# Kernel optimization log

Hardware: AMD Instinct MI355X
Metric: run time of the kernel (lower is better)

## Reference

```python
import jax, jax.numpy as jnp
import numpy as np

T, N, E = 12, 100000, 3200000
F = H = 64
O, L = 32, 2


def setup_inputs() -> dict:
    key = jax.random.key(0)
    ks = jax.random.split(key, 13)
    sc = 0.08  # keep gate pre-activations in a sane range
    return {
        "x": jax.random.normal(ks[0], (T, N, F), jnp.float32),
        "hidden_states": jax.random.normal(ks[1], (L, N, H), jnp.float32),
        "cell_states": jax.random.normal(ks[2], (L, N, H), jnp.float32),
        "Wx_self": jax.random.normal(ks[3], (L, 4, F, H), jnp.float32) * sc,
        "Wx_neigh": jax.random.normal(ks[4], (L, 4, F, H), jnp.float32) * sc,
        "Wh_self": jax.random.normal(ks[5], (L, 4, H, H), jnp.float32) * sc,
        "Wh_neigh": jax.random.normal(ks[6], (L, 4, H, H), jnp.float32) * sc,
        "w_c": jax.random.normal(ks[7], (L, 3, H), jnp.float32) * sc,  # peephole i,f,o
        "bias": jax.random.normal(ks[8], (L, 4, H), jnp.float32) * sc,  # i,f,c,o
        "Wout": jax.random.normal(ks[9], (H, O), jnp.float32) * sc,
        "bout": jax.random.normal(ks[10], (O,), jnp.float32) * sc,
        "src": jax.random.randint(ks[11], (E,), 0, N, jnp.int32),
        "dst": jax.random.randint(ks[12], (E,), 0, N, jnp.int32),
    }


def reference(x, hidden_states, cell_states, Wx_self, Wx_neigh, Wh_self,
              Wh_neigh, w_c, bias, Wout, bout, src, dst):
    # mean aggregation over incoming edges (DGL copy_u + mean reduce)
    deg = jax.ops.segment_sum(jnp.ones((E,), x.dtype), dst, num_segments=N)
    deg_inv = jnp.where(deg > 0, 1.0 / deg, 0.0)[:, None]  # [N,1]

    def mean_agg(feat):  # [N,D] -> [N,D]
        return jax.ops.segment_sum(feat[src], dst, num_segments=N) * deg_inv

    def gates(feat, agg, Ws, Wn):  # Ws,Wn: [4,D,H] -> [4,N,H]
        return (jnp.einsum('nf,gfh->gnh', feat, Ws)
                + jnp.einsum('nf,gfh->gnh', agg, Wn))

    def step(carry, x_t):
        hs, cs = carry  # [L,N,H] each
        inp = x_t
        new_h, new_c = [], []
        for j in range(L):
            h, c = hs[j], cs[j]
            x_agg = mean_agg(inp)  # reuse_msg_passing: one agg shared by 4 gates
            h_agg = mean_agg(h)
            pre = gates(inp, x_agg, Wx_self[j], Wx_neigh[j]) \
                + gates(h, h_agg, Wh_self[j], Wh_neigh[j])  # [4,N,H]
            i = jax.nn.sigmoid(pre[0] + w_c[j, 0] * c + bias[j, 0])
            f = jax.nn.sigmoid(pre[1] + w_c[j, 1] * c + bias[j, 1])
            c_tilde = jnp.tanh(pre[2] + bias[j, 2])
            nc = f * c + i * c_tilde
            o = jax.nn.sigmoid(pre[3] + w_c[j, 2] * nc + bias[j, 3])
            nh = o * jnp.tanh(nc)
            new_h.append(nh)
            new_c.append(nc)
            inp = nh
        out_t = inp @ Wout + bout  # [N,O]
        return (jnp.stack(new_h), jnp.stack(new_c)), out_t

    (h_f, c_f), outs = jax.lax.scan(step, (hidden_states, cell_states), x)
    return outs, h_f, c_f  # outs: [T,N,O]
```

## Files before the change

kernel.cpp:

```cpp
#include <hip/hip_runtime.h>

#define T_STEPS 12
#define NN 100000
#define EE 3200000
#define HD 64
#define OD 32
#define NBK 391

typedef __attribute__((ext_vector_type(8))) short short8;
typedef __attribute__((ext_vector_type(4))) float f32x4;
typedef __attribute__((ext_vector_type(2))) float f32x2;
typedef unsigned short u16;
typedef unsigned char u8;

__device__ __forceinline__ u16 f2b(float x) {
  union { float f; unsigned u; } v; v.f = x;
  unsigned r = v.u + 0x7FFFu + ((v.u >> 16) & 1u);
  return (u16)(r >> 16);
}
__device__ __forceinline__ float sigm(float x) {
  x = fminf(fmaxf(x, -30.f), 30.f);
  return 1.0f / (1.0f + __expf(-x));
}
__device__ __forceinline__ float tanh_f(float x) {
  x = fminf(fmaxf(x, -15.f), 15.f);
  float e = __expf(2.0f * x);
  return (e - 1.0f) / (e + 1.0f);
}

__device__ __forceinline__ uint2 pack8_fp8(const float* f) {
  unsigned lo = 0, hi = 0;
  lo = __builtin_amdgcn_cvt_pk_fp8_f32(f[0], f[1], lo, false);
  lo = __builtin_amdgcn_cvt_pk_fp8_f32(f[2], f[3], lo, true);
  hi = __builtin_amdgcn_cvt_pk_fp8_f32(f[4], f[5], hi, false);
  hi = __builtin_amdgcn_cvt_pk_fp8_f32(f[6], f[7], hi, true);
  return make_uint2(lo, hi);
}
__device__ __forceinline__ u8 f2q(float x) {
  return (u8)(__builtin_amdgcn_cvt_pk_fp8_f32(x, 0.f, 0u, false) & 0xFFu);
}
__device__ __forceinline__ void acc8_fp8(uint2 v, float* a) {
  f32x2 p0 = __builtin_amdgcn_cvt_pk_f32_fp8(v.x, false);
  f32x2 p1 = __builtin_amdgcn_cvt_pk_f32_fp8(v.x, true);
  f32x2 p2 = __builtin_amdgcn_cvt_pk_f32_fp8(v.y, false);
  f32x2 p3 = __builtin_amdgcn_cvt_pk_f32_fp8(v.y, true);
  a[0] += p0[0]; a[1] += p0[1]; a[2] += p1[0]; a[3] += p1[1];
  a[4] += p2[0]; a[5] += p2[1]; a[6] += p3[0]; a[7] += p3[1];
}
__device__ __forceinline__ void dec16_acc(uint4 q, float* a) {
  f32x2 t;
  t = __builtin_amdgcn_cvt_pk_f32_fp8(q.x, false); a[0] += t[0]; a[1] += t[1];
  t = __builtin_amdgcn_cvt_pk_f32_fp8(q.x, true);  a[2] += t[0]; a[3] += t[1];
  t = __builtin_amdgcn_cvt_pk_f32_fp8(q.y, false); a[4] += t[0]; a[5] += t[1];
  t = __builtin_amdgcn_cvt_pk_f32_fp8(q.y, true);  a[6] += t[0]; a[7] += t[1];
  t = __builtin_amdgcn_cvt_pk_f32_fp8(q.z, false); a[8] += t[0]; a[9] += t[1];
  t = __builtin_amdgcn_cvt_pk_f32_fp8(q.z, true);  a[10] += t[0]; a[11] += t[1];
  t = __builtin_amdgcn_cvt_pk_f32_fp8(q.w, false); a[12] += t[0]; a[13] += t[1];
  t = __builtin_amdgcn_cvt_pk_f32_fp8(q.w, true);  a[14] += t[0]; a[15] += t[1];
}
__device__ __forceinline__ short8 s8_from_fp8(uint2 q) {
  f32x2 p0 = __builtin_amdgcn_cvt_pk_f32_fp8(q.x, false);
  f32x2 p1 = __builtin_amdgcn_cvt_pk_f32_fp8(q.x, true);
  f32x2 p2 = __builtin_amdgcn_cvt_pk_f32_fp8(q.y, false);
  f32x2 p3 = __builtin_amdgcn_cvt_pk_f32_fp8(q.y, true);
  short8 o;
  o[0] = (short)f2b(p0[0]); o[1] = (short)f2b(p0[1]);
  o[2] = (short)f2b(p1[0]); o[3] = (short)f2b(p1[1]);
  o[4] = (short)f2b(p2[0]); o[5] = (short)f2b(p2[1]);
  o[6] = (short)f2b(p3[0]); o[7] = (short)f2b(p3[1]);
  return o;
}
__device__ __forceinline__ short8 s8_from_f32(float4 a, float4 b) {
  short8 o;
  o[0] = (short)f2b(a.x); o[1] = (short)f2b(a.y);
  o[2] = (short)f2b(a.z); o[3] = (short)f2b(a.w);
  o[4] = (short)f2b(b.x); o[5] = (short)f2b(b.y);
  o[6] = (short)f2b(b.z); o[7] = (short)f2b(b.w);
  return o;
}

__global__ __launch_bounds__(256) void k_bhist(const int* __restrict__ dst,
                                               int* __restrict__ bcnt, int E) {
  __shared__ int h[NBK];
  for (int i = threadIdx.x; i < NBK; i += 256) h[i] = 0;
  __syncthreads();
  int base = blockIdx.x * 4096;
#pragma unroll
  for (int i = 0; i < 16; ++i) {
    int e = base + i * 256 + threadIdx.x;
    if (e < E) atomicAdd(&h[dst[e] >> 8], 1);
  }
  __syncthreads();
  for (int i = threadIdx.x; i < NBK; i += 256)
    if (h[i]) atomicAdd(&bcnt[i], h[i]);
}

__global__ __launch_bounds__(512) void k_bscan(const int* __restrict__ bcnt,
                                               int* __restrict__ bcur) {
  __shared__ int buf[512];
  int tid = threadIdx.x;
  int v = (tid < NBK) ? bcnt[tid] : 0;
  buf[tid] = v;
  __syncthreads();
  for (int off = 1; off < 512; off <<= 1) {
    int t = (tid >= off) ? buf[tid - off] : 0;
    __syncthreads();
    buf[tid] += t;
    __syncthreads();
  }
  if (tid < NBK) bcur[tid] = buf[tid] - v;
}

__global__ __launch_bounds__(256) void k_bscatter(const int* __restrict__ src,
                                                  const int* __restrict__ dst,
                                                  int* __restrict__ bcur,
                                                  uint2* __restrict__ binned, int E) {
  __shared__ int h[NBK];
  __shared__ int base[NBK];
  __shared__ int cur[NBK];
  for (int i = threadIdx.x; i < NBK; i += 256) { h[i] = 0; cur[i] = 0; }
  __syncthreads();
  int b0 = blockIdx.x * 4096;
  int d[16], s[16];
#pragma unroll
  for (int i = 0; i < 16; ++i) {
    int e = b0 + i * 256 + threadIdx.x;
    if (e < E) {
      d[i] = dst[e];
      s[i] = src[e];
      atomicAdd(&h[d[i] >> 8], 1);
    } else d[i] = -1;
  }
  __syncthreads();
  for (int i = threadIdx.x; i < NBK; i += 256)
    if (h[i]) base[i] = atomicAdd(&bcur[i], h[i]);
  __syncthreads();
#pragma unroll
  for (int i = 0; i < 16; ++i) {
    if (d[i] >= 0) {
      int bk = d[i] >> 8;
      int r = atomicAdd(&cur[bk], 1);
      binned[base[bk] + r] = make_uint2((unsigned)s[i], (unsigned)d[i]);
    }
  }
}

__global__ __launch_bounds__(256) void k_count2(const uint2* __restrict__ binned,
                                                int* __restrict__ deg, int E) {
  int e = blockIdx.x * 256 + threadIdx.x;
  if (e < E) atomicAdd(&deg[binned[e].y], 1);
}

__global__ __launch_bounds__(1024) void k_scanA(const int* __restrict__ deg,
                                                int* __restrict__ excl,
                                                int* __restrict__ btot, int n) {
  __shared__ int buf[1024];
  int tid = threadIdx.x;
  int i = blockIdx.x * 1024 + tid;
  int v = (i < n) ? deg[i] : 0;
  buf[tid] = v;
  __syncthreads();
  for (int off = 1; off < 1024; off <<= 1) {
    int t = (tid >= off) ? buf[tid - off] : 0;
    __syncthreads();
    buf[tid] += t;
    __syncthreads();
  }
  if (i < n) excl[i] = buf[tid] - v;
  if (tid == 1023) btot[blockIdx.x] = buf[1023];
}

__global__ __launch_bounds__(128) void k_scanB(const int* __restrict__ btot,
                                               int* __restrict__ boffs, int nb) {
  __shared__ int buf[128];
  int tid = threadIdx.x;
  int v = (tid < nb) ? btot[tid] : 0;
  buf[tid] = v;
  __syncthreads();
  for (int off = 1; off < 128; off <<= 1) {
    int t = (tid >= off) ? buf[tid - off] : 0;
    __syncthreads();
    buf[tid] += t;
    __syncthreads();
  }
  if (tid < nb) boffs[tid] = buf[tid] - v;
}

__global__ __launch_bounds__(1024) void k_scanC(const int* __restrict__ deg,
                                                const int* __restrict__ excl,
                                                const int* __restrict__ boffs,
                                                int* __restrict__ row_ptr,
                                                int* __restrict__ cursor,
                                                float* __restrict__ deg_inv, int n) {
  int i = blockIdx.x * 1024 + threadIdx.x;
  if (i < n) {
    int v = excl[i] + boffs[blockIdx.x];
    int d = deg[i];
    row_ptr[i] = v;
    cursor[i] = v;
    deg_inv[i] = d ? (1.0f / (float)d) : 0.0f;
    if (i == n - 1) row_ptr[n] = v + d;
  }
}

__global__ __launch_bounds__(256) void k_scatter2(const uint2* __restrict__ binned,
                                                  int* __restrict__ cursor,
                                                  int* __restrict__ csr, int E) {
  int e = blockIdx.x * 256 + threadIdx.x;
  if (e < E) {
    uint2 p = binned[e];
    int pos = atomicAdd(&cursor[p.y], 1);
    csr[pos] = (int)p.x;
  }
}

__global__ __launch_bounds__(256) void k_prep(const float* __restrict__ Wxs,
                                              const float* __restrict__ Wxn,
                                              const float* __restrict__ Whs,
                                              const float* __restrict__ Whn,
                                              u16* __restrict__ bprep) {
  int idx = blockIdx.x * 256 + threadIdx.x;
  int l = idx >> 16;
  int kb = (idx >> 13) & 7;
  int fi = (idx >> 9) & 15;
  int ln = (idx >> 3) & 63;
  int j = idx & 7;
  int fc = kb * 32 + ((ln >> 4) << 3) + j;
  int g = fi & 3;
  int kk = ((fi >> 2) << 4) + (ln & 15);
  int t = fc >> 6, f = fc & 63;
  const float* tabs[4] = {Wxs, Wxn, Whs, Whn};
  bprep[idx] = f2b(tabs[t][((size_t)(l * 4 + g) * 64 + f) * 64 + kk]);
}

__global__ __launch_bounds__(256) void k_prepw(const float* __restrict__ Wout,
                                               u16* __restrict__ wp) {
  int idx = blockIdx.x * 256 + threadIdx.x;
  int kb = idx >> 10;
  int fi = (idx >> 9) & 1;
  int ln = (idx >> 3) & 63;
  int j = idx & 7;
  int k = kb * 32 + ((ln >> 4) << 3) + j;
  int o = fi * 16 + (ln & 15);
  wp[idx] = f2b(Wout[k * 32 + o]);
}

__global__ __launch_bounds__(256) void k_convxall(const float* __restrict__ x,
                                                  u8* __restrict__ XQ) {
  int tid = blockIdx.x * 256 + threadIdx.x;
  int j = tid & 7;
  int tn = tid >> 3;
  int n = tn % NN;
  int t = tn / NN;
  const float* rp = x + (size_t)tn * 64 + j * 8;
  float4 v0 = *reinterpret_cast<const float4*>(rp);
  float4 v1 = *reinterpret_cast<const float4*>(rp + 4);
  float f[8] = {v0.x, v0.y, v0.z, v0.w, v1.x, v1.y, v1.z, v1.w};
  *reinterpret_cast<uint2*>(XQ + (size_t)n * 768 + t * 64 + j * 8) = pack8_fp8(f);
}

__global__ __launch_bounds__(256) void k_inith(const float* __restrict__ h0,
                                               u16* __restrict__ H0bf,
                                               u16* __restrict__ L1bf,
                                               u8* __restrict__ HQ) {
  int idx = blockIdx.x * 256 + threadIdx.x;
  int n = idx >> 3, j = idx & 7;
#pragma unroll
  for (int L = 0; L < 2; ++L) {
    const float* rp = h0 + (size_t)L * NN * 64 + (size_t)n * 64 + j * 8;
    float4 v0 = *reinterpret_cast<const float4*>(rp);
    float4 v1 = *reinterpret_cast<const float4*>(rp + 4);
    float f[8] = {v0.x, v0.y, v0.z, v0.w, v1.x, v1.y, v1.z, v1.w};
    short8 o;
#pragma unroll
    for (int i = 0; i < 8; ++i) o[i] = (short)f2b(f[i]);
    if (L == 0)
      *reinterpret_cast<short8*>(H0bf + (size_t)n * 64 + j * 8) = o;
    else
      *reinterpret_cast<short8*>(L1bf + (size_t)n * 64 + j * 8) = o;
    *reinterpret_cast<uint2*>(HQ + (size_t)n * 128 + L * 64 + j * 8) = pack8_fp8(f);
  }
}

__global__ __launch_bounds__(256) void k_aggx(const u8* __restrict__ XQ,
                                              const int* __restrict__ row_ptr,
                                              const int* __restrict__ csr,
                                              const float* __restrict__ deg_inv,
                                              u8* __restrict__ AGGXq) {
  int node = blockIdx.x * 4 + (threadIdx.x >> 6);
  int lane = threadIdx.x & 63;
  int g = lane >> 4, m = lane & 15;
  int start = row_ptr[node], end = row_ptr[node + 1];
  float acc[3][16];
#pragma unroll
  for (int p = 0; p < 3; ++p)
#pragma unroll
    for (int i = 0; i < 16; ++i) acc[p][i] = 0.f;
  int e = start + g;
  for (; e + 4 < end; e += 8) {
    int s0 = csr[e], s1 = csr[e + 4];
    const u8* r0 = XQ + (size_t)s0 * 768 + m * 16;
    const u8* r1 = XQ + (size_t)s1 * 768 + m * 16;
#pragma unroll
    for (int p = 0; p < 3; ++p) {
      uint4 q0 = *reinterpret_cast<const uint4*>(r0 + p * 256);
      uint4 q1 = *reinterpret_cast<const uint4*>(r1 + p * 256);
      dec16_acc(q0, acc[p]);
      dec16_acc(q1, acc[p]);
    }
  }
  if (e < end) {
    int s0 = csr[e];
    const u8* r0 = XQ + (size_t)s0 * 768 + m * 16;
#pragma unroll
    for (int p = 0; p < 3; ++p) {
      uint4 q0 = *reinterpret_cast<const uint4*>(r0 + p * 256);
      dec16_acc(q0, acc[p]);
    }
  }
#pragma unroll
  for (int off = 16; off < 64; off <<= 1)
#pragma unroll
    for (int p = 0; p < 3; ++p)
#pragma unroll
      for (int i = 0; i < 16; ++i) acc[p][i] += __shfl_xor(acc[p][i], off);
  if (g == 0) {
    float sc = deg_inv[node];
#pragma unroll
    for (int p = 0; p < 3; ++p) {
      float f[16];
#pragma unroll
      for (int i = 0; i < 16; ++i) f[i] = acc[p][i] * sc;
      uint4 o;
      unsigned w;
      w = 0; w = __builtin_amdgcn_cvt_pk_fp8_f32(f[0], f[1], w, false);
      w = __builtin_amdgcn_cvt_pk_fp8_f32(f[2], f[3], w, true); o.x = w;
      w = 0; w = __builtin_amdgcn_cvt_pk_fp8_f32(f[4], f[5], w, false);
      w = __builtin_amdgcn_cvt_pk_fp8_f32(f[6], f[7], w, true); o.y = w;
      w = 0; w = __builtin_amdgcn_cvt_pk_fp8_f32(f[8], f[9], w, false);
      w = __builtin_amdgcn_cvt_pk_fp8_f32(f[10], f[11], w, true); o.z = w;
      w = 0; w = __builtin_amdgcn_cvt_pk_fp8_f32(f[12], f[13], w, false);
      w = __builtin_amdgcn_cvt_pk_fp8_f32(f[14], f[15], w, true); o.w = w;
      int t = p * 4 + (m >> 2);
      *reinterpret_cast<uint4*>(AGGXq + ((size_t)t * NN + node) * 64 + (m & 3) * 16) = o;
    }
  }
}

__global__ __launch_bounds__(256) void k_agg_pair(const u8* __restrict__ Q,
                                                  const int* __restrict__ row_ptr,
                                                  const int* __restrict__ csr,
                                                  const float* __restrict__ deg_inv,
                                                  u16* __restrict__ outp) {
  int node = blockIdx.x * 4 + (threadIdx.x >> 6);
  int lane = threadIdx.x & 63;
  int g = lane >> 4, m = lane & 15;
  int start = row_ptr[node], end = row_ptr[node + 1];
  float a[8] = {0, 0, 0, 0, 0, 0, 0, 0};
  int e = start + g;
  for (; e + 12 < end; e += 16) {
    int s0 = csr[e], s1 = csr[e + 4], s2 = csr[e + 8], s3 = csr[e + 12];
    uint2 v0 = *reinterpret_cast<const uint2*>(Q + (size_t)s0 * 128 + m * 8);
    uint2 v1 = *reinterpret_cast<const uint2*>(Q + (size_t)s1 * 128 + m * 8);
    uint2 v2 = *reinterpret_cast<const uint2*>(Q + (size_t)s2 * 128 + m * 8);
    uint2 v3 = *reinterpret_cast<const uint2*>(Q + (size_t)s3 * 128 + m * 8);
    acc8_fp8(v0, a); acc8_fp8(v1, a); acc8_fp8(v2, a); acc8_fp8(v3, a);
  }
  if (e + 4 < end) {
    int s0 = csr[e], s1 = csr[e + 4];
    uint2 v0 = *reinterpret_cast<const uint2*>(Q + (size_t)s0 * 128 + m * 8);
    uint2 v1 = *reinterpret_cast<const uint2*>(Q + (size_t)s1 * 128 + m * 8);
    acc8_fp8(v0, a); acc8_fp8(v1, a);
    e += 8;
  }
  if (e < end) {
    int s0 = csr[e];
    uint2 v0 = *reinterpret_cast<const uint2*>(Q + (size_t)s0 * 128 + m * 8);
    acc8_fp8(v0, a);
  }
#pragma unroll
  for (int off = 16; off < 64; off <<= 1) {
#pragma unroll
    for (int i = 0; i < 8; ++i) a[i] += __shfl_xor(a[i], off);
  }
  if (g == 0) {
    float sc = deg_inv[node];
    short8 o;
#pragma unroll
    for (int i = 0; i < 8; ++i) o[i] = (short)f2b(a[i] * sc);
    *reinterpret_cast<short8*>(outp + (size_t)node * 128 + m * 8) = o;
  }
}

__global__ __launch_bounds__(256, 2) void k_gates0(
    const float* __restrict__ xin, const u8* __restrict__ aggxq,
    u16* __restrict__ h0bf, const u16* __restrict__ agghl,
    u8* __restrict__ hq, float* __restrict__ cst, float* __restrict__ hf32,
    const u16* __restrict__ bprepl,
    const float* __restrict__ wcl, const float* __restrict__ biasl,
    int n_nodes, int writef32) {
  const int tid = threadIdx.x;
  const int lane = tid & 63;
  const int w = tid >> 6;
  const int nb = blockIdx.x * 64;
  const int cl = lane & 15;
  const int kg = lane >> 4;

  short8 breg[8][4];
#pragma unroll
  for (int kb = 0; kb < 8; ++kb)
#pragma unroll
    for (int fl = 0; fl < 4; ++fl)
      breg[kb][fl] = *reinterpret_cast<const short8*>(
          bprepl + (kb << 13) + (((w << 2) + fl) << 9) + (lane << 3));

  int gnc[4];
#pragma unroll
  for (int rg = 0; rg < 4; ++rg) {
    int g = nb + rg * 16 + cl;
    gnc[rg] = (g < n_nodes) ? g : (n_nodes - 1);
  }

  f32x4 acc[4][4];
  f32x4 z4 = {0.f, 0.f, 0.f, 0.f};
#pragma unroll
  for (int a = 0; a < 4; ++a)
#pragma unroll
    for (int b = 0; b < 4; ++b) acc[a][b] = z4;

  const int koff = kg << 3;
#pragma unroll
  for (int kb = 0; kb < 8; ++kb) {
    const int idx = ((kb & 1) << 5) + koff;
#pragma unroll
    for (int rg = 0; rg < 4; ++rg) {
      short8 a;
      if (kb < 2) {
        const float* rp = xin + (size_t)gnc[rg] * 64 + idx;
        a = s8_from_f32(*reinterpret_cast<const float4*>(rp),
                        *reinterpret_cast<const float4*>(rp + 4));
      } else if (kb < 4) {
        a = s8_from_fp8(*reinterpret_cast<const uint2*>(aggxq + (size_t)gnc[rg] * 64 + idx));
      } else if (kb < 6) {
        a = *reinterpret_cast<const short8*>(h0bf + (size_t)gnc[rg] * 64 + idx);
      } else {
        a = *reinterpret_cast<const short8*>(agghl + (size_t)gnc[rg] * 128 + idx);
      }
      acc[rg][0] = __builtin_amdgcn_mfma_f32_16x16x32_bf16(a, breg[kb][0], acc[rg][0], 0, 0, 0);
      acc[rg][1] = __builtin_amdgcn_mfma_f32_16x16x32_bf16(a, breg[kb][1], acc[rg][1], 0, 0, 0);
      acc[rg][2] = __builtin_amdgcn_mfma_f32_16x16x32_bf16(a, breg[kb][2], acc[rg][2], 0, 0, 0);
      acc[rg][3] = __builtin_amdgcn_mfma_f32_16x16x32_bf16(a, breg[kb][3], acc[rg][3], 0, 0, 0);
    }
  }

  const int k = (w << 4) + cl;
  const float wci = wcl[k], wcf = wcl[64 + k], wco = wcl[128 + k];
  const float bi = biasl[k], bfg = biasl[64 + k], bc = biasl[128 + k], bo = biasl[192 + k];
#pragma unroll
  for (int rg = 0; rg < 4; ++rg) {
#pragma unroll
    for (int r = 0; r < 4; ++r) {
      int n = nb + rg * 16 + kg * 4 + r;
      if (n < n_nodes) {
        size_t off = (size_t)n * 64 + k;
        float c_old = cst[off];
        float ig = sigm(acc[rg][0][r] + wci * c_old + bi);
        float fg = sigm(acc[rg][1][r] + wcf * c_old + bfg);
        float ct = tanh_f(acc[rg][2][r] + bc);
        float nc = fg * c_old + ig * ct;
        float og = sigm(acc[rg][3][r] + wco * nc + bo);
        float nh = og * tanh_f(nc);
        cst[off] = nc;
        h0bf[off] = f2b(nh);
        hq[(size_t)n * 128 + k] = f2q(nh);
        if (writef32) hf32[off] = nh;
      }
    }
  }
}

__global__ __launch_bounds__(256, 2) void k_gates1(
    const u16* __restrict__ h0bf, const u16* __restrict__ agghl,
    u16* __restrict__ l1bf, u8* __restrict__ hq,
    float* __restrict__ cst, float* __restrict__ hf32,
    const u16* __restrict__ bprepl,
    const float* __restrict__ wcl, const float* __restrict__ biasl,
    const u16* __restrict__ wproj, const float* __restrict__ boutp,
    float* __restrict__ outp, int n_nodes, int writef32) {
  __shared__ u16 Hsm[64 * 64];
  const int tid = threadIdx.x;
  const int lane = tid & 63;
  const int w = tid >> 6;
  const int nb = blockIdx.x * 64;
  const int cl = lane & 15;
  const int kg = lane >> 4;

  short8 breg[8][4];
#pragma unroll
  for (int kb = 0; kb < 8; ++kb)
#pragma unroll
    for (int fl = 0; fl < 4; ++fl)
      breg[kb][fl] = *reinterpret_cast<const short8*>(
          bprepl + (kb << 13) + (((w << 2) + fl) << 9) + (lane << 3));

  int gnc[4];
#pragma unroll
  for (int rg = 0; rg < 4; ++rg) {
    int g = nb + rg * 16 + cl;
    gnc[rg] = (g < n_nodes) ? g : (n_nodes - 1);
  }

  f32x4 acc[4][4];
  f32x4 z4 = {0.f, 0.f, 0.f, 0.f};
#pragma unroll
  for (int a = 0; a < 4; ++a)
#pragma unroll
    for (int b = 0; b < 4; ++b) acc[a][b] = z4;

  const int koff = kg << 3;
#pragma unroll
  for (int kb = 0; kb < 8; ++kb) {
    const int idx = ((kb & 1) << 5) + koff;
#pragma unroll
    for (int rg = 0; rg < 4; ++rg) {
      short8 a;
      if (kb < 2) {
        a = *reinterpret_cast<const short8*>(h0bf + (size_t)gnc[rg] * 64 + idx);
      } else if (kb < 4) {
        a = *reinterpret_cast<const short8*>(agghl + (size_t)gnc[rg] * 128 + idx);
      } else if (kb < 6) {
        a = *reinterpret_cast<const short8*>(l1bf + (size_t)gnc[rg] * 64 + idx);
      } else {
        a = *reinterpret_cast<const short8*>(agghl + (size_t)gnc[rg] * 128 + 64 + idx);
      }
      acc[rg][0] = __builtin_amdgcn_mfma_f32_16x16x32_bf16(a, breg[kb][0], acc[rg][0], 0, 0, 0);
      acc[rg][1] = __builtin_amdgcn_mfma_f32_16x16x32_bf16(a, breg[kb][1], acc[rg][1], 0, 0, 0);
      acc[rg][2] = __builtin_amdgcn_mfma_f32_16x16x32_bf16(a, breg[kb][2], acc[rg][2], 0, 0, 0);
      acc[rg][3] = __builtin_amdgcn_mfma_f32_16x16x32_bf16(a, breg[kb][3], acc[rg][3], 0, 0, 0);
    }
  }

  const int k = (w << 4) + cl;
  const float wci = wcl[k], wcf = wcl[64 + k], wco = wcl[128 + k];
  const float bi = biasl[k], bfg = biasl[64 + k], bc = biasl[128 + k], bo = biasl[192 + k];
#pragma unroll
  for (int rg = 0; rg < 4; ++rg) {
#pragma unroll
    for (int r = 0; r < 4; ++r) {
      int n = nb + rg * 16 + kg * 4 + r;
      if (n < n_nodes) {
        size_t off = (size_t)n * 64 + k;
        float c_old = cst[off];
        float ig = sigm(acc[rg][0][r] + wci * c_old + bi);
        float fg = sigm(acc[rg][1][r] + wcf * c_old + bfg);
        float ct = tanh_f(acc[rg][2][r] + bc);
        float nc = fg * c_old + ig * ct;
        float og = sigm(acc[rg][3][r] + wco * nc + bo);
        float nh = og * tanh_f(nc);
        cst[off] = nc;
        u16 hb = f2b(nh);
        l1bf[off] = hb;
        hq[(size_t)n * 128 + 64 + k] = f2q(nh);
        Hsm[(rg * 16 + kg * 4 + r) * 64 + k] = hb;
        if (writef32) hf32[off] = nh;
      }
    }
  }

  __syncthreads();
  short8 bw[2][2];
#pragma unroll
  for (int kb = 0; kb < 2; ++kb)
#pragma unroll
    for (int fi = 0; fi < 2; ++fi)
      bw[kb][fi] = *reinterpret_cast<const short8*>(wproj + (((kb * 2 + fi) * 64 + lane) << 3));
  short8 a0 = *reinterpret_cast<const short8*>(&Hsm[(w * 16 + cl) * 64 + kg * 8]);
  short8 a1 = *reinterpret_cast<const short8*>(&Hsm[(w * 16 + cl) * 64 + 32 + kg * 8]);
  f32x4 p0 = z4, p1 = z4;
  p0 = __builtin_amdgcn_mfma_f32_16x16x32_bf16(a0, bw[0][0], p0, 0, 0, 0);
  p0 = __builtin_amdgcn_mfma_f32_16x16x32_bf16(a1, bw[1][0], p0, 0, 0, 0);
  p1 = __builtin_amdgcn_mfma_f32_16x16x32_bf16(a0, bw[0][1], p1, 0, 0, 0);
  p1 = __builtin_amdgcn_mfma_f32_16x16x32_bf16(a1, bw[1][1], p1, 0, 0, 0);
  const float bo0 = boutp[cl], bo1 = boutp[16 + cl];
#pragma unroll
  for (int r = 0; r < 4; ++r) {
    int n = nb + w * 16 + kg * 4 + r;
    if (n < n_nodes) {
      outp[(size_t)n * OD + cl] = p0[r] + bo0;
      outp[(size_t)n * OD + 16 + cl] = p1[r] + bo1;
    }
  }
}

extern "C" void kernel_launch(void* const* d_in, const int* in_sizes, int n_in,
                              void* d_out, int out_size, void* d_ws, size_t ws_size,
                              hipStream_t stream) {
  const float* x = (const float*)d_in[0];
  const float* h0 = (const float*)d_in[1];
  const float* c0 = (const float*)d_in[2];
  const float* Wxs = (const float*)d_in[3];
  const float* Wxn = (const float*)d_in[4];
  const float* Whs = (const float*)d_in[5];
  const float* Whn = (const float*)d_in[6];
  const float* wc = (const float*)d_in[7];
  const float* bias = (const float*)d_in[8];
  const float* Wout = (const float*)d_in[9];
  const float* bout = (const float*)d_in[10];
  const int* src = (const int*)d_in[11];
  const int* dst = (const int*)d_in[12];

  float* out = (float*)d_out;
  float* outs = out;
  float* hstate = out + (size_t)T_STEPS * NN * OD;
  float* cstate = hstate + (size_t)2 * NN * HD;

  char* p = (char*)d_ws;
  auto alloc = [&](size_t bytes) {
    char* r = p;
    p += (bytes + 255) & ~(size_t)255;
    return r;
  };
  int* csr = (int*)alloc((size_t)EE * 4);
  u8* XQ = (u8*)alloc((size_t)NN * 768);
  uint2* binned = (uint2*)XQ;
  u8* AGGXq = (u8*)alloc((size_t)T_STEPS * NN * 64);
  int* row_ptr = (int*)alloc((size_t)(NN + 1) * 4);
  int* cursor = (int*)alloc((size_t)NN * 4);
  int* deg = (int*)alloc((size_t)NN * 4);
  int* excl = (int*)alloc((size_t)NN * 4);
  int* btot = (int*)alloc(128 * 4);
  int* boffs = (int*)alloc(128 * 4);
  int* bcnt = (int*)alloc(NBK * 4);
  int* bcur = (int*)alloc(NBK * 4);
  float* deg_inv = (float*)alloc((size_t)NN * 4);
  u16* H0bf = (u16*)alloc((size_t)NN * 64 * 2);
  u16* L1bf = (u16*)alloc((size_t)NN * 64 * 2);
  u8* HQ = (u8*)alloc((size_t)NN * 128);
  u16* AGGHL = (u16*)alloc((size_t)NN * 128 * 2);
  u16* bprep = (u16*)alloc((size_t)2 * 65536 * 2);
  u16* wprep = (u16*)alloc((size_t)2048 * 2);

  const int nscan = (NN + 1023) / 1024;
  const int nchunk = (EE + 4095) / 4096;

  hipMemsetAsync(deg, 0, (size_t)NN * 4, stream);
  hipMemsetAsync(bcnt, 0, (size_t)NBK * 4, stream);
  k_bhist<<<nchunk, 256, 0, stream>>>(dst, bcnt, EE);
  k_bscan<<<1, 512, 0, stream>>>(bcnt, bcur);
  k_bscatter<<<nchunk, 256, 0, stream>>>(src, dst, bcur, binned, EE);
  k_count2<<<(EE + 255) / 256, 256, 0, stream>>>(binned, deg, EE);
  k_scanA<<<nscan, 1024, 0, stream>>>(deg, excl, btot, NN);
  k_scanB<<<1, 128, 0, stream>>>(btot, boffs, nscan);
  k_scanC<<<nscan, 1024, 0, stream>>>(deg, excl, boffs, row_ptr, cursor, deg_inv, NN);
  k_scatter2<<<(EE + 255) / 256, 256, 0, stream>>>(binned, cursor, csr, EE);
  k_prep<<<512, 256, 0, stream>>>(Wxs, Wxn, Whs, Whn, bprep);
  k_prepw<<<8, 256, 0, stream>>>(Wout, wprep);
  k_convxall<<<(T_STEPS * NN * 8 + 255) / 256, 256, 0, stream>>>(x, XQ);
  k_inith<<<NN * 8 / 256, 256, 0, stream>>>(h0, H0bf, L1bf, HQ);
  hipMemcpyAsync(cstate, c0, (size_t)2 * NN * HD * 4, hipMemcpyDeviceToDevice, stream);
  k_aggx<<<(NN + 3) / 4, 256, 0, stream>>>(XQ, row_ptr, csr, deg_inv, AGGXq);
  k_agg_pair<<<(NN + 3) / 4, 256, 0, stream>>>(HQ, row_ptr, csr, deg_inv, AGGHL);

  for (int t = 0; t < T_STEPS; ++t) {
    int wf = (t == T_STEPS - 1) ? 1 : 0;
    k_gates0<<<(NN + 63) / 64, 256, 0, stream>>>(
        x + (size_t)t * NN * HD, AGGXq + (size_t)t * NN * 64,
        H0bf, AGGHL, HQ, cstate, hstate, bprep, wc, bias, NN, wf);
    k_agg_pair<<<(NN + 3) / 4, 256, 0, stream>>>(HQ, row_ptr, csr, deg_inv, AGGHL);
    k_gates1<<<(NN + 63) / 64, 256, 0, stream>>>(
        H0bf, AGGHL, L1bf, HQ,
        cstate + (size_t)NN * HD, hstate + (size_t)NN * HD,
        bprep + 65536, wc + 192, bias + 256,
        wprep, bout, outs + (size_t)t * NN * OD, NN, wf);
  }
}
```

Baseline: 2.998 ms.

## Store cell state in fp16, split agg buffer, use packed fp8 accumulation

Keeps the recurrent cell state in a half-precision buffer between steps, so the per-step gate kernels read and write 2 bytes per element instead of 4. The fp32 state is written only on the last step, and the initial copy becomes a conversion inside the init kernel. The aggregated hidden buffer is split into two contiguous per-layer arrays. The x-aggregation accumulates in packed float2 vectors so packed adds can be used. A block barrier is also inserted after the MFMA loop. Storing the cell state in fp16 adds rounding error that builds up over the 12 recurrent steps.

```diff
diff --git a/kernel.cpp b/kernel.cpp
--- a/kernel.cpp
+++ b/kernel.cpp
@@ -17,6 +17,12 @@
   union { float f; unsigned u; } v; v.f = x;
   unsigned r = v.u + 0x7FFFu + ((v.u >> 16) & 1u);
   return (u16)(r >> 16);
+}
+__device__ __forceinline__ u16 f2h(float x) {
+  union { _Float16 h; u16 s; } u; u.h = (_Float16)x; return u.s;
+}
+__device__ __forceinline__ float h2f(u16 s) {
+  union { u16 s; _Float16 h; } u; u.s = s; return (float)u.h;
 }
 __device__ __forceinline__ float sigm(float x) {
   x = fminf(fmaxf(x, -30.f), 30.f);
@@ -47,16 +53,15 @@
   a[0] += p0[0]; a[1] += p0[1]; a[2] += p1[0]; a[3] += p1[1];
   a[4] += p2[0]; a[5] += p2[1]; a[6] += p3[0]; a[7] += p3[1];
 }
-__device__ __forceinline__ void dec16_acc(uint4 q, float* a) {
-  f32x2 t;
-  t = __builtin_amdgcn_cvt_pk_f32_fp8(q.x, false); a[0] += t[0]; a[1] += t[1];
-  t = __builtin_amdgcn_cvt_pk_f32_fp8(q.x, true);  a[2] += t[0]; a[3] += t[1];
-  t = __builtin_amdgcn_cvt_pk_f32_fp8(q.y, false); a[4] += t[0]; a[5] += t[1];
-  t = __builtin_amdgcn_cvt_pk_f32_fp8(q.y, true);  a[6] += t[0]; a[7] += t[1];
-  t = __builtin_amdgcn_cvt_pk_f32_fp8(q.z, false); a[8] += t[0]; a[9] += t[1];
-  t = __builtin_amdgcn_cvt_pk_f32_fp8(q.z, true);  a[10] += t[0]; a[11] += t[1];
-  t = __builtin_amdgcn_cvt_pk_f32_fp8(q.w, false); a[12] += t[0]; a[13] += t[1];
-  t = __builtin_amdgcn_cvt_pk_f32_fp8(q.w, true);  a[14] += t[0]; a[15] += t[1];
+__device__ __forceinline__ void dec16_acc2(uint4 q, f32x2* a) {
+  a[0] += __builtin_amdgcn_cvt_pk_f32_fp8(q.x, false);
+  a[1] += __builtin_amdgcn_cvt_pk_f32_fp8(q.x, true);
+  a[2] += __builtin_amdgcn_cvt_pk_f32_fp8(q.y, false);
+  a[3] += __builtin_amdgcn_cvt_pk_f32_fp8(q.y, true);
+  a[4] += __builtin_amdgcn_cvt_pk_f32_fp8(q.z, false);
+  a[5] += __builtin_amdgcn_cvt_pk_f32_fp8(q.z, true);
+  a[6] += __builtin_amdgcn_cvt_pk_f32_fp8(q.w, false);
+  a[7] += __builtin_amdgcn_cvt_pk_f32_fp8(q.w, true);
 }
 __device__ __forceinline__ short8 s8_from_fp8(uint2 q) {
   f32x2 p0 = __builtin_amdgcn_cvt_pk_f32_fp8(q.x, false);
@@ -260,9 +265,11 @@
 }
 
 __global__ __launch_bounds__(256) void k_inith(const float* __restrict__ h0,
+                                               const float* __restrict__ c0,
                                                u16* __restrict__ H0bf,
                                                u16* __restrict__ L1bf,
-                                               u8* __restrict__ HQ) {
+                                               u8* __restrict__ HQ,
+                                               u16* __restrict__ C16) {
   int idx = blockIdx.x * 256 + threadIdx.x;
   int n = idx >> 3, j = idx & 7;
 #pragma unroll
@@ -279,6 +286,14 @@
     else
       *reinterpret_cast<short8*>(L1bf + (size_t)n * 64 + j * 8) = o;
     *reinterpret_cast<uint2*>(HQ + (size_t)n * 128 + L * 64 + j * 8) = pack8_fp8(f);
+    const float* cp = c0 + (size_t)L * NN * 64 + (size_t)n * 64 + j * 8;
+    float4 c0v = *reinterpret_cast<const float4*>(cp);
+    float4 c1v = *reinterpret_cast<const float4*>(cp + 4);
+    float cf[8] = {c0v.x, c0v.y, c0v.z, c0v.w, c1v.x, c1v.y, c1v.z, c1v.w};
+    short8 oc;
+#pragma unroll
+    for (int i = 0; i < 8; ++i) oc[i] = (short)f2h(cf[i]);
+    *reinterpret_cast<short8*>(C16 + (size_t)L * NN * 64 + (size_t)n * 64 + j * 8) = oc;
   }
 }
 
@@ -291,11 +306,11 @@
   int lane = threadIdx.x & 63;
   int g = lane >> 4, m = lane & 15;
   int start = row_ptr[node], end = row_ptr[node + 1];
-  float acc[3][16];
+  f32x2 acc[3][8];
 #pragma unroll
   for (int p = 0; p < 3; ++p)
 #pragma unroll
-    for (int i = 0; i < 16; ++i) acc[p][i] = 0.f;
+    for (int i = 0; i < 8; ++i) acc[p][i] = (f32x2){0.f, 0.f};
   int e = start + g;
   for (; e + 4 < end; e += 8) {
     int s0 = csr[e], s1 = csr[e + 4];
@@ -305,8 +320,8 @@
     for (int p = 0; p < 3; ++p) {
       uint4 q0 = *reinterpret_cast<const uint4*>(r0 + p * 256);
       uint4 q1 = *reinterpret_cast<const uint4*>(r1 + p * 256);
-      dec16_acc(q0, acc[p]);
-      dec16_acc(q1, acc[p]);
+      dec16_acc2(q0, acc[p]);
+      dec16_acc2(q1, acc[p]);
     }
   }
   if (e < end) {
@@ -315,7 +330,7 @@
 #pragma unroll
     for (int p = 0; p < 3; ++p) {
       uint4 q0 = *reinterpret_cast<const uint4*>(r0 + p * 256);
-      dec16_acc(q0, acc[p]);
+      dec16_acc2(q0, acc[p]);
     }
   }
 #pragma unroll
@@ -323,14 +338,20 @@
 #pragma unroll
     for (int p = 0; p < 3; ++p)
 #pragma unroll
-      for (int i = 0; i < 16; ++i) acc[p][i] += __shfl_xor(acc[p][i], off);
+      for (int i = 0; i < 8; ++i) {
+        acc[p][i][0] += __shfl_xor(acc[p][i][0], off);
+        acc[p][i][1] += __shfl_xor(acc[p][i][1], off);
+      }
   if (g == 0) {
     float sc = deg_inv[node];
 #pragma unroll
     for (int p = 0; p < 3; ++p) {
       float f[16];
 #pragma unroll
-      for (int i = 0; i < 16; ++i) f[i] = acc[p][i] * sc;
+      for (int i = 0; i < 8; ++i) {
+        f[i * 2] = acc[p][i][0] * sc;
+        f[i * 2 + 1] = acc[p][i][1] * sc;
+      }
       uint4 o;
       unsigned w;
       w = 0; w = __builtin_amdgcn_cvt_pk_fp8_f32(f[0], f[1], w, false);
@@ -351,7 +372,8 @@
                                                   const int* __restrict__ row_ptr,
                                                   const int* __restrict__ csr,
                                                   const float* __restrict__ deg_inv,
-                                                  u16* __restrict__ outp) {
+                                                  u16* __restrict__ out0,
+                                                  u16* __restrict__ out1) {
   int node = blockIdx.x * 4 + (threadIdx.x >> 6);
   int lane = threadIdx.x & 63;
   int g = lane >> 4, m = lane & 15;
@@ -388,17 +410,21 @@
     short8 o;
 #pragma unroll
     for (int i = 0; i < 8; ++i) o[i] = (short)f2b(a[i] * sc);
-    *reinterpret_cast<short8*>(outp + (size_t)node * 128 + m * 8) = o;
+    if (m < 8)
+      *reinterpret_cast<short8*>(out0 + (size_t)node * 64 + m * 8) = o;
+    else
+      *reinterpret_cast<short8*>(out1 + (size_t)node * 64 + (m - 8) * 8) = o;
   }
 }
 
 __global__ __launch_bounds__(256, 2) void k_gates0(
     const float* __restrict__ xin, const u8* __restrict__ aggxq,
-    u16* __restrict__ h0bf, const u16* __restrict__ agghl,
-    u8* __restrict__ hq, float* __restrict__ cst, float* __restrict__ hf32,
+    u16* __restrict__ h0bf, const u16* __restrict__ aggh0,
+    u8* __restrict__ hq, u16* __restrict__ c16,
+    float* __restrict__ hf32, float* __restrict__ cf32,
     const u16* __restrict__ bprepl,
     const float* __restrict__ wcl, const float* __restrict__ biasl,
-    int n_nodes, int writef32) {
+    int n_nodes, int wf) {
   const int tid = threadIdx.x;
   const int lane = tid & 63;
   const int w = tid >> 6;
@@ -444,7 +470,7 @@
       } else if (kb < 6) {
         a = *reinterpret_cast<const short8*>(h0bf + (size_t)gnc[rg] * 64 + idx);
       } else {
-        a = *reinterpret_cast<const short8*>(agghl + (size_t)gnc[rg] * 128 + idx);
+        a = *reinterpret_cast<const short8*>(aggh0 + (size_t)gnc[rg] * 64 + idx);
       }
       acc[rg][0] = __builtin_amdgcn_mfma_f32_16x16x32_bf16(a, breg[kb][0], acc[rg][0], 0, 0, 0);
       acc[rg][1] = __builtin_amdgcn_mfma_f32_16x16x32_bf16(a, breg[kb][1], acc[rg][1], 0, 0, 0);
@@ -452,6 +478,7 @@
       acc[rg][3] = __builtin_amdgcn_mfma_f32_16x16x32_bf16(a, breg[kb][3], acc[rg][3], 0, 0, 0);
     }
   }
+  __syncthreads();
 
   const int k = (w << 4) + cl;
   const float wci = wcl[k], wcf = wcl[64 + k], wco = wcl[128 + k];
@@ -463,30 +490,31 @@
       int n = nb + rg * 16 + kg * 4 + r;
       if (n < n_nodes) {
         size_t off = (size_t)n * 64 + k;
-        float c_old = cst[off];
+        float c_old = h2f(c16[off]);
         float ig = sigm(acc[rg][0][r] + wci * c_old + bi);
         float fg = sigm(acc[rg][1][r] + wcf * c_old + bfg);
         float ct = tanh_f(acc[rg][2][r] + bc);
         float nc = fg * c_old + ig * ct;
         float og = sigm(acc[rg][3][r] + wco * nc + bo);
         float nh = og * tanh_f(nc);
-        cst[off] = nc;
+        c16[off] = f2h(nc);
         h0bf[off] = f2b(nh);
         hq[(size_t)n * 128 + k] = f2q(nh);
-        if (writef32) hf32[off] = nh;
+        if (wf) { hf32[off] = nh; cf32[off] = nc; }
       }
     }
   }
 }
 
 __global__ __launch_bounds__(256, 2) void k_gates1(
-    const u16* __restrict__ h0bf, const u16* __restrict__ agghl,
-    u16* __restrict__ l1bf, u8* __restrict__ hq,
-    float* __restrict__ cst, float* __restrict__ hf32,
+    const u16* __restrict__ h0bf, const u16* __restrict__ aggh0,
+    const u16* __restrict__ aggh1,
+    u16* __restrict__ l1bf, u8* __restrict__ hq, u16* __restrict__ c16,
+    float* __restrict__ hf32, float* __restrict__ cf32,
     const u16* __restrict__ bprepl,
     const float* __restrict__ wcl, const float* __restrict__ biasl,
     const u16* __restrict__ wproj, const float* __restrict__ boutp,
-    float* __restrict__ outp, int n_nodes, int writef32) {
+    float* __restrict__ outp, int n_nodes, int wf) {
   __shared__ u16 Hsm[64 * 64];
   const int tid = threadIdx.x;
   const int lane = tid & 63;
@@ -527,11 +555,11 @@
       if (kb < 2) {
         a = *reinterpret_cast<const short8*>(h0bf + (size_t)gnc[rg] * 64 + idx);
       } else if (kb < 4) {
-        a = *reinterpret_cast<const short8*>(agghl + (size_t)gnc[rg] * 128 + idx);
+        a = *reinterpret_cast<const short8*>(aggh0 + (size_t)gnc[rg] * 64 + idx);
       } else if (kb < 6) {
         a = *reinterpret_cast<const short8*>(l1bf + (size_t)gnc[rg] * 64 + idx);
       } else {
-        a = *reinterpret_cast<const short8*>(agghl + (size_t)gnc[rg] * 128 + 64 + idx);
+        a = *reinterpret_cast<const short8*>(aggh1 + (size_t)gnc[rg] * 64 + idx);
       }
       acc[rg][0] = __builtin_amdgcn_mfma_f32_16x16x32_bf16(a, breg[kb][0], acc[rg][0], 0, 0, 0);
       acc[rg][1] = __builtin_amdgcn_mfma_f32_16x16x32_bf16(a, breg[kb][1], acc[rg][1], 0, 0, 0);
@@ -539,6 +567,7 @@
       acc[rg][3] = __builtin_amdgcn_mfma_f32_16x16x32_bf16(a, breg[kb][3], acc[rg][3], 0, 0, 0);
     }
   }
+  __syncthreads();
 
   const int k = (w << 4) + cl;
   const float wci = wcl[k], wcf = wcl[64 + k], wco = wcl[128 + k];
@@ -550,19 +579,19 @@
       int n = nb + rg * 16 + kg * 4 + r;
       if (n < n_nodes) {
         size_t off = (size_t)n * 64 + k;
-        float c_old = cst[off];
+        float c_old = h2f(c16[off]);
         float ig = sigm(acc[rg][0][r] + wci * c_old + bi);
         float fg = sigm(acc[rg][1][r] + wcf * c_old + bfg);
         float ct = tanh_f(acc[rg][2][r] + bc);
         float nc = fg * c_old + ig * ct;
         float og = sigm(acc[rg][3][r] + wco * nc + bo);
         float nh = og * tanh_f(nc);
-        cst[off] = nc;
+        c16[off] = f2h(nc);
         u16 hb = f2b(nh);
         l1bf[off] = hb;
         hq[(size_t)n * 128 + 64 + k] = f2q(nh);
         Hsm[(rg * 16 + kg * 4 + r) * 64 + k] = hb;
-        if (writef32) hf32[off] = nh;
+        if (wf) { hf32[off] = nh; cf32[off] = nc; }
       }
     }
   }
@@ -636,7 +665,9 @@
   u16* H0bf = (u16*)alloc((size_t)NN * 64 * 2);
   u16* L1bf = (u16*)alloc((size_t)NN * 64 * 2);
   u8* HQ = (u8*)alloc((size_t)NN * 128);
-  u16* AGGHL = (u16*)alloc((size_t)NN * 128 * 2);
+  u16* AGGH0 = (u16*)alloc((size_t)NN * 64 * 2);
+  u16* AGGH1 = (u16*)alloc((size_t)NN * 64 * 2);
+  u16* C16 = (u16*)alloc((size_t)2 * NN * 64 * 2);
   u16* bprep = (u16*)alloc((size_t)2 * 65536 * 2);
   u16* wprep = (u16*)alloc((size_t)2048 * 2);
 
@@ -656,20 +687,19 @@
   k_prep<<<512, 256, 0, stream>>>(Wxs, Wxn, Whs, Whn, bprep);
   k_prepw<<<8, 256, 0, stream>>>(Wout, wprep);
   k_convxall<<<(T_STEPS * NN * 8 + 255) / 256, 256, 0, stream>>>(x, XQ);
-  k_inith<<<NN * 8 / 256, 256, 0, stream>>>(h0, H0bf, L1bf, HQ);
-  hipMemcpyAsync(cstate, c0, (size_t)2 * NN * HD * 4, hipMemcpyDeviceToDevice, stream);
+  k_inith<<<NN * 8 / 256, 256, 0, stream>>>(h0, c0, H0bf, L1bf, HQ, C16);
   k_aggx<<<(NN + 3) / 4, 256, 0, stream>>>(XQ, row_ptr, csr, deg_inv, AGGXq);
-  k_agg_pair<<<(NN + 3) / 4, 256, 0, stream>>>(HQ, row_ptr, csr, deg_inv, AGGHL);
+  k_agg_pair<<<(NN + 3) / 4, 256, 0, stream>>>(HQ, row_ptr, csr, deg_inv, AGGH0, AGGH1);
 
   for (int t = 0; t < T_STEPS; ++t) {
     int wf = (t == T_STEPS - 1) ? 1 : 0;
     k_gates0<<<(NN + 63) / 64, 256, 0, stream>>>(
         x + (size_t)t * NN * HD, AGGXq + (size_t)t * NN * 64,
-        H0bf, AGGHL, HQ, cstate, hstate, bprep, wc, bias, NN, wf);
-    k_agg_pair<<<(NN + 3) / 4, 256, 0, stream>>>(HQ, row_ptr, csr, deg_inv, AGGHL);
+        H0bf, AGGH0, HQ, C16, hstate, cstate, bprep, wc, bias, NN, wf);
+    k_agg_pair<<<(NN + 3) / 4, 256, 0, stream>>>(HQ, row_ptr, csr, deg_inv, AGGH0, AGGH1);
     k_gates1<<<(NN + 63) / 64, 256, 0, stream>>>(
-        H0bf, AGGHL, L1bf, HQ,
-        cstate + (size_t)NN * HD, hstate + (size_t)NN * HD,
+        H0bf, AGGH0, AGGH1, L1bf, HQ, C16 + (size_t)NN * 64,
+        hstate + (size_t)NN * HD, cstate + (size_t)NN * HD,
         bprep + 65536, wc + 192, bias + 256,
         wprep, bout, outs + (size_t)t * NN * OD, NN, wf);
   }
```

After: 2.984 ms. Within noise of the previous version (-0.5%).
